# Performance work log

Hardware: AMD Instinct MI355X
Metric: run time of the kernel (lower is better)

The kernel has to match this reference:

```python
import jax, jax.numpy as jnp
import numpy as np

N = 8192          # number of atoms
N_ELEM = 95       # r2r4 table size (elements 0..94)
EPS = 1e-12


def setup_inputs() -> dict:
    key = jax.random.key(0)
    k1, k2, k3 = jax.random.split(key, 3)
    atomic_numbers = jax.random.randint(k1, (N,), 0, N_ELEM)
    # positions in a ~60 Angstrom box so pair distances are realistic
    positions = jax.random.uniform(k2, (N, 3), dtype=jnp.float32) * 60.0
    r2r4 = jax.random.uniform(k3, (N_ELEM,), dtype=jnp.float32)
    # Becke-Johnson damping parameters (PBE D3-BJ)
    a1 = jnp.float32(0.4289)
    a2 = jnp.float32(4.4407)
    s6 = jnp.float32(1.0)
    s8 = jnp.float32(0.7875)
    return {"atomic_numbers": atomic_numbers, "positions": positions,
            "r2r4": r2r4, "a1": a1, "a2": a2, "s6": s6, "s8": s8}


def reference(atomic_numbers, positions, r2r4, a1, a2, s6, s8):
    # Per-atom-type gather (present in source; mathematically unused because
    # the source hard-codes c6 = c8 = 1 via all-ones LazyTensors).
    r2r4_z = r2r4[atomic_numbers]                      # (N,)

    # All-pairs squared distances. d appears only as d^6 and d^8, which are
    # polynomials in d2, so no sqrt is needed (also keeps diagonal smooth).
    diff = positions[:, None, :] - positions[None, :, :]   # (N, N, 3)
    d2 = jnp.sum(diff * diff, axis=-1)                     # (N, N)
    d6 = d2 * d2 * d2
    d8 = d6 * d2

    # c6 = c8 = 1  =>  tmp = a1 * sqrt(c8/c6) + a2 = a1 + a2
    tmp = a1 + a2
    tmp2 = tmp * tmp
    tmp6 = tmp2 * tmp2 * tmp2
    tmp8 = tmp6 * tmp2

    c6 = jnp.float32(1.0)
    c8 = jnp.float32(1.0)
    D_ij = -s6 * c6 / (d6 + tmp6 + EPS) - s8 * c8 / (d8 + tmp8 + EPS)

    # mask d > eps  <=>  d2 > eps^2 (removes self-terms)
    mask = d2 > EPS * EPS
    D_ij = jnp.where(mask, D_ij, jnp.float32(0.0))

    # a_i = sum_j D_ij ; energy = sum_i a_i
    return jnp.sum(D_ij) + jnp.float32(0.0) * jnp.sum(r2r4_z)
```

## Files before the change

### kernel.cpp

```cpp
#include <hip/hip_runtime.h>

#define NA 8192
#define IT 128
#define JT 64
#define NI (NA / IT)
#define NJ (NA / JT)
#define NJOB 4160
#define WPB 8
#define BLOCK (WPB * 64)
#define NBLK (NJOB / WPB)
#define S_OF(I) ((I) * (129 - (I)))

typedef float v2f __attribute__((ext_vector_type(2)));

__device__ __forceinline__ float bcast(float v, int k) {
    return __int_as_float(__builtin_amdgcn_readlane(__float_as_int(v), k));
}

__global__ __launch_bounds__(BLOCK, 4) void dftd3_pair_energy(
    const float* __restrict__ pos,
    const float* __restrict__ p_a1, const float* __restrict__ p_a2,
    const float* __restrict__ p_s6, const float* __restrict__ p_s8,
    float* __restrict__ partial, int* __restrict__ cnt,
    float* __restrict__ out)
{
    const int tid  = threadIdx.x;
    const int lane = tid & 63;
    const int w = __builtin_amdgcn_readfirstlane(blockIdx.x * WPB + (tid >> 6));

    int I = (int)((129.0f - sqrtf(16641.0f - 4.0f * (float)w)) * 0.5f);
    if (I < 0) I = 0;
    if (I > NI - 1) I = NI - 1;
    while (S_OF(I + 1) <= w) ++I;
    while (S_OF(I) > w) --I;
    const int J = 2 * I + (w - S_OF(I));
    const bool edge = (w - S_OF(I)) < 2;

    const int j = J * JT + lane;
    const float vxj = pos[3 * j + 0];
    const float vyj = pos[3 * j + 1];
    const float vzj = pos[3 * j + 2];

    const int i0 = I * IT + 2 * lane;
    const v2f xi = { pos[3 * i0 + 0], pos[3 * i0 + 3] };
    const v2f yi = { pos[3 * i0 + 1], pos[3 * i0 + 4] };
    const v2f zi = { pos[3 * i0 + 2], pos[3 * i0 + 5] };

    const float a1 = p_a1[0], a2 = p_a2[0];
    const float s6 = p_s6[0], s8 = p_s8[0];
    const float tmp  = a1 + a2;
    const float tmp2 = tmp * tmp;
    const float tmp6 = tmp2 * tmp2 * tmp2;
    const float tmp8 = tmp6 * tmp2;
    const float T6 = tmp6 + 1e-12f;
    const float T8 = tmp8 + 1e-12f;
    const float SC  = 3.5527137e-15f;
    const float ns6 = -s6 * SC;
    const float ns8 = -s8 * SC;

    float accx = 0.0f, accy = 0.0f;

    auto body = [&](int k, bool masked) {
        float sx = bcast(vxj, k);
        float sy = bcast(vyj, k);
        float sz = bcast(vzj, k);
        v2f dx = xi - sx;
        v2f dy = yi - sy;
        v2f dz = zi - sz;
        v2f d2 = __builtin_elementwise_fma(dx, dx,
                 __builtin_elementwise_fma(dy, dy, dz * dz));
        v2f d4 = d2 * d2;
        v2f A  = __builtin_elementwise_fma(d4, d2, (v2f)T6);
        v2f B  = __builtin_elementwise_fma(d4, d4, (v2f)T8);
        v2f num = __builtin_elementwise_fma((v2f)ns6, B, (v2f)ns8 * A);
        v2f den = A * B;
        v2f dens = den * (v2f)SC;
        float t = dens.x * dens.y;
        float r = __builtin_amdgcn_rcpf(t);
        float numx = num.x, numy = num.y;
        if (masked) {
            const int jk = J * JT + k;
            numx = (jk > i0)     ? numx : 0.0f;
            numy = (jk > i0 + 1) ? numy : 0.0f;
        }
        accx = fmaf(numx, dens.y * r, accx);
        accy = fmaf(numy, dens.x * r, accy);
    };

    if (edge) {
        #pragma unroll 8
        for (int k = 0; k < JT; ++k) body(k, true);
    } else {
        #pragma unroll 8
        for (int k = 0; k < JT; ++k) body(k, false);
    }

    float acc = 2.0f * (accx + accy);

    #pragma unroll
    for (int off = 32; off > 0; off >>= 1)
        acc += __shfl_xor(acc, off, 64);

    __shared__ float wsum[WPB];
    __shared__ int lastflag;
    if (lane == 0) wsum[tid >> 6] = acc;
    __syncthreads();
    if (tid == 0) {
        float s = 0.0f;
        #pragma unroll
        for (int q = 0; q < WPB; ++q) s += wsum[q];
        atomicExch(&partial[blockIdx.x], s);
        __threadfence();
        int old = atomicAdd(cnt, 1);
        lastflag = (old == NBLK - 1);
    }
    __syncthreads();
    if (lastflag) {
        __threadfence();
        float s = 0.0f;
        for (int t = tid; t < NBLK; t += BLOCK)
            s += atomicAdd(&partial[t], 0.0f);
        #pragma unroll
        for (int off = 32; off > 0; off >>= 1)
            s += __shfl_xor(s, off, 64);
        if (lane == 0) wsum[tid >> 6] = s;
        __syncthreads();
        if (tid == 0) {
            float tot = 0.0f;
            #pragma unroll
            for (int q = 0; q < WPB; ++q) tot += wsum[q];
            out[0] = tot;
        }
    }
}

extern "C" void kernel_launch(void* const* d_in, const int* in_sizes, int n_in,
                              void* d_out, int out_size, void* d_ws, size_t ws_size,
                              hipStream_t stream) {
    const float* pos = (const float*)d_in[1];
    const float* a1  = (const float*)d_in[3];
    const float* a2  = (const float*)d_in[4];
    const float* s6  = (const float*)d_in[5];
    const float* s8  = (const float*)d_in[6];
    float* partial = (float*)d_ws;
    int*   cnt     = (int*)((char*)d_ws + 65536);
    float* out     = (float*)d_out;

    hipMemsetAsync(cnt, 0, sizeof(int), stream);

    dftd3_pair_energy<<<dim3(NBLK), BLOCK, 0, stream>>>(pos, a1, a2, s6, s8,
                                                        partial, cnt, out);
}
```

Baseline: 87.61 us.

## Rebalance pair work into 4096 equal 65-body wave chunks with LDS j-tiles

Instead of one 64-body job per wave (4160 waves, 520 blocks), the triangular job list is flattened and split into 4096 contiguous chunks of 65 bodies. Each wave may span two adjacent j-tiles, and possibly two i-tiles. The grid becomes 512 blocks, which divides evenly over the CUs and aims to remove the tail of a partial last wave of blocks. The per-j broadcasts now come from a per-wave LDS tile read as a float4, replacing readlane from VGPRs. This adds tile-boundary logic and LDS traffic, and swapping the loop mid-wave adds some extra setup cost.

Result: faster. 84.60 us (-3.4%).

```diff
diff --git a/kernel.cpp b/kernel.cpp
--- a/kernel.cpp
+++ b/kernel.cpp
@@ -4,18 +4,17 @@
 #define IT 128
 #define JT 64
 #define NI (NA / IT)
-#define NJ (NA / JT)
 #define NJOB 4160
+#define NBODY (NJOB * JT)
+#define NWAVE 4096
+#define BPW 65
 #define WPB 8
 #define BLOCK (WPB * 64)
-#define NBLK (NJOB / WPB)
+#define NBLK (NWAVE / WPB)
 #define S_OF(I) ((I) * (129 - (I)))
 
 typedef float v2f __attribute__((ext_vector_type(2)));
-
-__device__ __forceinline__ float bcast(float v, int k) {
-    return __int_as_float(__builtin_amdgcn_readlane(__float_as_int(v), k));
-}
+typedef float v4f __attribute__((ext_vector_type(4)));
 
 __global__ __launch_bounds__(BLOCK, 4) void dftd3_pair_energy(
     const float* __restrict__ pos,
@@ -26,25 +25,12 @@
 {
     const int tid  = threadIdx.x;
     const int lane = tid & 63;
-    const int w = __builtin_amdgcn_readfirstlane(blockIdx.x * WPB + (tid >> 6));
+    const int wv   = tid >> 6;
+    const int q = __builtin_amdgcn_readfirstlane(blockIdx.x * WPB + wv);
 
-    int I = (int)((129.0f - sqrtf(16641.0f - 4.0f * (float)w)) * 0.5f);
-    if (I < 0) I = 0;
-    if (I > NI - 1) I = NI - 1;
-    while (S_OF(I + 1) <= w) ++I;
-    while (S_OF(I) > w) --I;
-    const int J = 2 * I + (w - S_OF(I));
-    const bool edge = (w - S_OF(I)) < 2;
-
-    const int j = J * JT + lane;
-    const float vxj = pos[3 * j + 0];
-    const float vyj = pos[3 * j + 1];
-    const float vzj = pos[3 * j + 2];
-
-    const int i0 = I * IT + 2 * lane;
-    const v2f xi = { pos[3 * i0 + 0], pos[3 * i0 + 3] };
-    const v2f yi = { pos[3 * i0 + 1], pos[3 * i0 + 4] };
-    const v2f zi = { pos[3 * i0 + 2], pos[3 * i0 + 5] };
+    __shared__ v4f jtile[WPB][JT];
+    __shared__ float wsum[WPB];
+    __shared__ int lastflag;
 
     const float a1 = p_a1[0], a2 = p_a2[0];
     const float s6 = p_s6[0], s8 = p_s8[0];
@@ -58,15 +44,39 @@
     const float ns6 = -s6 * SC;
     const float ns8 = -s8 * SC;
 
-    float accx = 0.0f, accy = 0.0f;
+    const int b0   = q * BPW;
+    const int jobA = b0 >> 6;
+    const int kA   = b0 & 63;
+
+    int I = (int)((129.0f - sqrtf(16641.0f - 4.0f * (float)jobA)) * 0.5f);
+    if (I < 0) I = 0;
+    if (I > NI - 1) I = NI - 1;
+    while (S_OF(I + 1) <= jobA) ++I;
+    while (S_OF(I) > jobA) --I;
+    int J = 2 * I + (jobA - S_OF(I));
+
+    v2f xi, yi, zi;
+    int i0 = 0;
+    int Jbase = 0;
+
+    auto load_i = [&](int It) {
+        i0 = It * IT + 2 * lane;
+        xi = (v2f){ pos[3 * i0 + 0], pos[3 * i0 + 3] };
+        yi = (v2f){ pos[3 * i0 + 1], pos[3 * i0 + 4] };
+        zi = (v2f){ pos[3 * i0 + 2], pos[3 * i0 + 5] };
+    };
+    auto stage_j = [&](int Jt) {
+        int j = Jt * JT + lane;
+        jtile[wv][lane] = (v4f){ pos[3 * j + 0], pos[3 * j + 1], pos[3 * j + 2], 0.0f };
+    };
+
+    v2f acc = {0.0f, 0.0f};
 
     auto body = [&](int k, bool masked) {
-        float sx = bcast(vxj, k);
-        float sy = bcast(vyj, k);
-        float sz = bcast(vzj, k);
-        v2f dx = xi - sx;
-        v2f dy = yi - sy;
-        v2f dz = zi - sz;
+        v4f pj = jtile[wv][k];
+        v2f dx = xi - pj.x;
+        v2f dy = yi - pj.y;
+        v2f dz = zi - pj.z;
         v2f d2 = __builtin_elementwise_fma(dx, dx,
                  __builtin_elementwise_fma(dy, dy, dz * dz));
         v2f d4 = d2 * d2;
@@ -77,38 +87,49 @@
         v2f dens = den * (v2f)SC;
         float t = dens.x * dens.y;
         float r = __builtin_amdgcn_rcpf(t);
-        float numx = num.x, numy = num.y;
         if (masked) {
-            const int jk = J * JT + k;
-            numx = (jk > i0)     ? numx : 0.0f;
-            numy = (jk > i0 + 1) ? numy : 0.0f;
+            int jk = Jbase + k;
+            num.x = (jk > i0)     ? num.x : 0.0f;
+            num.y = (jk > i0 + 1) ? num.y : 0.0f;
         }
-        accx = fmaf(numx, dens.y * r, accx);
-        accy = fmaf(numy, dens.x * r, accy);
+        v2f rec = __builtin_shufflevector(dens, dens, 1, 0) * r;
+        acc = __builtin_elementwise_fma(num, rec, acc);
     };
 
-    if (edge) {
-        #pragma unroll 8
-        for (int k = 0; k < JT; ++k) body(k, true);
-    } else {
-        #pragma unroll 8
-        for (int k = 0; k < JT; ++k) body(k, false);
-    }
+    auto run = [&](int k0, int k1, bool edge) {
+        if (edge) {
+            #pragma unroll 8
+            for (int k = k0; k < k1; ++k) body(k, true);
+        } else {
+            #pragma unroll 8
+            for (int k = k0; k < k1; ++k) body(k, false);
+        }
+    };
 
-    float acc = 2.0f * (accx + accy);
+    load_i(I);
+    stage_j(J);
+    Jbase = J * JT;
+    run(kA, JT, (J - 2 * I) < 2);
+
+    int I2 = I, J2 = J + 1;
+    if (J == 127) { I2 = I + 1; J2 = 2 * I2; }
+    if (I2 != I) load_i(I2);
+    stage_j(J2);
+    Jbase = J2 * JT;
+    run(0, kA + 1, (J2 - 2 * I2) < 2);
+
+    float accs = 2.0f * (acc.x + acc.y);
 
     #pragma unroll
     for (int off = 32; off > 0; off >>= 1)
-        acc += __shfl_xor(acc, off, 64);
+        accs += __shfl_xor(accs, off, 64);
 
-    __shared__ float wsum[WPB];
-    __shared__ int lastflag;
-    if (lane == 0) wsum[tid >> 6] = acc;
+    if (lane == 0) wsum[wv] = accs;
     __syncthreads();
     if (tid == 0) {
         float s = 0.0f;
         #pragma unroll
-        for (int q = 0; q < WPB; ++q) s += wsum[q];
+        for (int p = 0; p < WPB; ++p) s += wsum[p];
         atomicExch(&partial[blockIdx.x], s);
         __threadfence();
         int old = atomicAdd(cnt, 1);
@@ -118,17 +139,17 @@
     if (lastflag) {
         __threadfence();
         float s = 0.0f;
-        for (int t = tid; t < NBLK; t += BLOCK)
-            s += atomicAdd(&partial[t], 0.0f);
+        for (int tt = tid; tt < NBLK; tt += BLOCK)
+            s += atomicAdd(&partial[tt], 0.0f);
         #pragma unroll
         for (int off = 32; off > 0; off >>= 1)
             s += __shfl_xor(s, off, 64);
-        if (lane == 0) wsum[tid >> 6] = s;
+        if (lane == 0) wsum[wv] = s;
         __syncthreads();
         if (tid == 0) {
             float tot = 0.0f;
             #pragma unroll
-            for (int q = 0; q < WPB; ++q) tot += wsum[q];
+            for (int p = 0; p < WPB; ++p) tot += wsum[p];
             out[0] = tot;
         }
     }
```
